# Kernel optimization log

Measured on AMD Instinct MI355X. Metric: run time of the kernel, lower is better.

The kernel has to match this reference:

```python
import jax, jax.numpy as jnp
import numpy as np

N, E, F_IN, HID, HEADS, C, NCLS, NG, NCONV = 50000, 800000, 128, 128, 8, 16, 10, 64, 3
EPS = 1e-5
NEG_SLOPE = 0.2


def bn_eval(x, p):
    # p: [4, dim] = (gamma, beta, running_mean, running_var); eval-mode BatchNorm1d
    g, b, m, v = p[0], p[1], p[2], p[3]
    return g * (x - m) * jax.lax.rsqrt(v + EPS) + b


def gat_conv(x, src, dst, W, a_src, a_dst, bias):
    # PyG GATConv, concat=True, add_self_loops=True, eval (no dropout)
    h = (x @ W).reshape(N, HEADS, C)                    # [N,H,C]
    alpha_s = jnp.sum(h * a_src[None], axis=-1)         # [N,H]
    alpha_d = jnp.sum(h * a_dst[None], axis=-1)         # [N,H]
    loop = jnp.arange(N)
    s = jnp.concatenate([src, loop])                    # [E+N]
    d = jnp.concatenate([dst, loop])
    logits = jax.nn.leaky_relu(alpha_s[s] + alpha_d[d], NEG_SLOPE)   # [E+N,H]
    mx = jax.lax.stop_gradient(jax.ops.segment_max(logits, d, num_segments=N))
    ex = jnp.exp(logits - mx[d])
    denom = jax.ops.segment_sum(ex, d, num_segments=N)
    alpha = ex / (denom[d] + 1e-16)                     # segment softmax over dst
    msg = h[s] * alpha[:, :, None]                      # [E+N,H,C]
    out = jax.ops.segment_sum(msg, d, num_segments=N)   # [N,H,C]
    return out.reshape(N, HEADS * C) + bias


def setup_inputs() -> dict:
    key = jax.random.key(0)
    ks = jax.random.split(key, 16)

    def bn_p(dim):
        return jnp.stack([jnp.ones(dim), jnp.full((dim,), 1e-4), jnp.zeros(dim), jnp.ones(dim)])

    sc = 0.05
    inp = {
        "x": jax.random.normal(ks[0], (N, F_IN), jnp.float32),
        "edge_index": jax.random.randint(ks[1], (2, E), 0, N),
        "batch": jnp.sort(jax.random.randint(ks[2], (N,), 0, NG)),
        "bn_feat_params": bn_p(F_IN),
        "w_feat": jax.random.normal(ks[3], (F_IN, HID), jnp.float32) * sc,
        "b_feat": jnp.zeros((HID,), jnp.float32),
        "bns_conv_params": jnp.stack([bn_p(HID)] * NCONV),
        "gat_w": jax.random.normal(ks[4], (NCONV, HID, HID), jnp.float32) * sc,
        "gat_att_src": jax.random.normal(ks[5], (NCONV, HEADS, C), jnp.float32) * sc,
        "gat_att_dst": jax.random.normal(ks[6], (NCONV, HEADS, C), jnp.float32) * sc,
        "gat_b": jnp.zeros((NCONV, HID), jnp.float32),
        "bns_fc_params": jnp.stack([bn_p(HID)] * 1),
        "fc_w": jax.random.normal(ks[7], (1, HID, HID), jnp.float32) * sc,
        "fc_b": jnp.zeros((1, HID), jnp.float32),
        "bn_hidden_params": bn_p(HID),
        "w_class": jax.random.normal(ks[8], (HID, NCLS), jnp.float32) * sc,
        "b_class": jnp.zeros((NCLS,), jnp.float32),
    }
    return inp


def reference(x, edge_index, batch, bn_feat_params, w_feat, b_feat, bns_conv_params,
              gat_w, gat_att_src, gat_att_dst, gat_b, bns_fc_params, fc_w, fc_b,
              bn_hidden_params, w_class, b_class):
    src, dst = edge_index[0], edge_index[1]
    h = bn_eval(x, bn_feat_params)
    h = jax.nn.relu(h @ w_feat + b_feat)             # GCNConv(gfn=True) == linear
    for i in range(NCONV):
        h = bn_eval(h, bns_conv_params[i])
        h = jax.nn.relu(gat_conv(h, src, dst, gat_w[i], gat_att_src[i], gat_att_dst[i], gat_b[i]))
    g = jax.ops.segment_sum(h, batch, num_segments=NG)   # global_add_pool -> [NG,HID]
    for i in range(fc_w.shape[0]):
        g = jax.nn.relu(bn_eval(g, bns_fc_params[i]) @ fc_w[i] + fc_b[i])
    g = bn_eval(g, bn_hidden_params)
    logits = g @ w_class + b_class
    return jax.nn.log_softmax(logits, axis=-1)
```

## Files before the change

kernel.cpp:

```cpp
#include <hip/hip_runtime.h>

#define NN 50000
#define E_EDGES 800000
#define F_INN 128
#define HIDD 128
#define HEADS 8
#define CDIM 16
#define NCLS 10
#define NGG 64
#define NCONV 3
#define EPSS 1e-5f
#define NEG_SLOPE 0.2f

#define WROWS 144
#define WSTRIDE (WROWS * 128)
#define BSTRIDE 144

#define BSH 7
#define BSZ 128
#define NB ((NN + BSZ - 1) / BSZ)
#define BIN_BLOCKS 256
#define BIN_CHUNK (E_EDGES / BIN_BLOCKS)
#define TABW 392
#define CAPB 4608
#define SORT_BUF 4608
#define PW_KCH 32
#define GTILES ((NN + 127) / 128)
#define TPITCH 132

typedef __attribute__((ext_vector_type(8))) short short8;
typedef __attribute__((ext_vector_type(4))) float f32x4;
typedef __attribute__((ext_vector_type(2))) float f32x2;

__device__ __forceinline__ float lrelu(float x) { return x > 0.f ? x : NEG_SLOPE * x; }

__device__ __forceinline__ float bf2f(ushort u) {
    union { unsigned int i; float f; } v;
    v.i = ((unsigned int)u) << 16;
    return v.f;
}
__device__ __forceinline__ ushort f2bf(float f) {
    union { float f; unsigned int i; } v;
    v.f = f;
    unsigned int r = (v.i + 0x7fffu + ((v.i >> 16) & 1u)) >> 16;
    return (ushort)r;
}
__device__ __forceinline__ unsigned char f2fp8(float f) {
    int r = __builtin_amdgcn_cvt_pk_fp8_f32(f, f, 0, false);
    return (unsigned char)(r & 0xff);
}

__device__ __forceinline__ void gemm_core_l0(int tile, int t,
    const float* __restrict__ Ain, const ushort* __restrict__ Wt,
    const float* __restrict__ bias, ushort* __restrict__ Out, int n)
{
    int wave = t >> 6, lane = t & 63;
    int m16 = lane & 15, quad = lane >> 4;
    int rbase = tile * 128 + wave * 32;

    short8 afrag[2][4];
    #pragma unroll
    for (int tt = 0; tt < 2; ++tt) {
        int arow_i = rbase + tt * 16 + m16;
        size_t arow = (size_t)(arow_i < n ? arow_i : 0) * HIDD + quad * 8;
        const float* ap = Ain + arow;
        #pragma unroll
        for (int kk = 0; kk < 4; ++kk) {
            float4 lo = *(const float4*)(ap + kk * 32);
            float4 hi = *(const float4*)(ap + kk * 32 + 4);
            short8 f;
            f[0] = (short)f2bf(lo.x); f[1] = (short)f2bf(lo.y);
            f[2] = (short)f2bf(lo.z); f[3] = (short)f2bf(lo.w);
            f[4] = (short)f2bf(hi.x); f[5] = (short)f2bf(hi.y);
            f[6] = (short)f2bf(hi.z); f[7] = (short)f2bf(hi.w);
            afrag[tt][kk] = f;
        }
    }

    f32x4 acc[2][8];
    #pragma unroll
    for (int tt = 0; tt < 2; ++tt)
        #pragma unroll
        for (int nt = 0; nt < 8; ++nt) acc[tt][nt] = (f32x4){0.f, 0.f, 0.f, 0.f};

    #pragma unroll
    for (int nt = 0; nt < 8; ++nt) {
        const ushort* brow = Wt + (size_t)(nt * 16 + m16) * HIDD + quad * 8;
        #pragma unroll
        for (int kk = 0; kk < 4; ++kk) {
            short8 bfrag = *(const short8*)(brow + kk * 32);
            acc[0][nt] = __builtin_amdgcn_mfma_f32_16x16x32_bf16(afrag[0][kk], bfrag, acc[0][nt], 0, 0, 0);
            acc[1][nt] = __builtin_amdgcn_mfma_f32_16x16x32_bf16(afrag[1][kk], bfrag, acc[1][nt], 0, 0, 0);
        }
    }

    #pragma unroll
    for (int tt = 0; tt < 2; ++tt) {
        int tb = rbase + tt * 16;
        #pragma unroll
        for (int nt = 0; nt < 8; ++nt) {
            int col = nt * 16 + m16;
            float bv = bias[col];
            #pragma unroll
            for (int r = 0; r < 4; ++r) {
                int orow = tb + quad * 4 + r;
                if (orow < n) {
                    float v = fmaxf(acc[tt][nt][r] + bv, 0.f);
                    Out[(size_t)orow * HIDD + col] = f2bf(v);
                }
            }
        }
    }
}

__global__ __launch_bounds__(256) void prep_bin(
    const float* __restrict__ bn_feat, const float* __restrict__ w_feat,
    const float* __restrict__ b_feat, const float* __restrict__ bns_conv,
    const float* __restrict__ gat_w, const float* __restrict__ att_src,
    const float* __restrict__ att_dst, const int* __restrict__ src,
    const int* __restrict__ dst, ushort* __restrict__ Wt,
    float* __restrict__ bp, unsigned int* __restrict__ tmp, int* __restrict__ tab)
{
    __shared__ __align__(16) char smem[18560];
    int blk = blockIdx.x;
    int t = threadIdx.x;

    if (blk < 16) {
        float* Wl = (float*)smem;
        float* aak = Wl + PW_KCH * 129;
        int layer = blk >> 2;
        int k0 = (blk & 3) * PW_KCH;
        const float* bn; const float* W;
        if (layer == 0) { bn = bn_feat; W = w_feat; }
        else { bn = bns_conv + (layer - 1) * 4 * HIDD; W = gat_w + (size_t)(layer - 1) * HIDD * HIDD; }
        if (t < PW_KCH) {
            int k = k0 + t;
            aak[t] = bn[k] * rsqrtf(bn[3 * HIDD + k] + EPSS);
        }
        for (int i = t; i < PW_KCH * 128; i += 256) {
            int kk = i >> 7, n = i & 127;
            Wl[kk * 129 + n] = W[(size_t)(k0 + kk) * 128 + n];
        }
        __syncthreads();
        ushort* wrow = Wt + (size_t)layer * WSTRIDE;
        for (int i = t; i < 128 * PW_KCH; i += 256) {
            int n = i >> 5, kk = i & 31;
            wrow[n * 128 + k0 + kk] = f2bf(aak[kk] * Wl[kk * 129 + n]);
        }
    } else if (blk < 20) {
        float* ccs = (float*)smem;
        int layer = blk - 16;
        const float* bn; const float* W;
        if (layer == 0) { bn = bn_feat; W = w_feat; }
        else { bn = bns_conv + (layer - 1) * 4 * HIDD; W = gat_w + (size_t)(layer - 1) * HIDD * HIDD; }
        if (t < 128) {
            float a = bn[t] * rsqrtf(bn[3 * HIDD + t] + EPSS);
            ccs[t] = bn[HIDD + t] - bn[2 * HIDD + t] * a;
        }
        __syncthreads();
        if (t < 128) {
            float bacc = (layer == 0) ? b_feat[t] : 0.f;
            for (int k = 0; k < 128; ++k) bacc += ccs[k] * W[(size_t)k * 128 + t];
            bp[layer * BSTRIDE + t] = bacc;
        }
    } else if (blk < 23) {
        float* Wl   = (float*)smem;
        float* redS = (float*)(smem + 16512);
        float* redD = redS + 256;
        int li = blk - 20;
        int L = li + 1;
        const float* bn = bns_conv + li * 4 * HIDD;
        const float* W  = gat_w + (size_t)li * HIDD * HIDD;
        const float* as = att_src + li * HEADS * CDIM;
        const float* ad = att_dst + li * HEADS * CDIM;
        ushort* Wo = Wt + (size_t)L * WSTRIDE;
        int kl = t >> 3, h = t & 7;
        float acc_s = 0.f, acc_d = 0.f;
        for (int c0 = 0; c0 < 4; ++c0) {
            int k0 = c0 * 32;
            __syncthreads();
            for (int i = t; i < 32 * 128; i += 256) {
                int kk = i >> 7, n = i & 127;
                Wl[kk * 129 + n] = W[(size_t)(k0 + kk) * 128 + n];
            }
            __syncthreads();
            int k = k0 + kl;
            float a  = bn[k] * rsqrtf(bn[3 * HIDD + k] + EPSS);
            float cc = bn[HIDD + k] - bn[2 * HIDD + k] * a;
            float ps = 0.f, pd = 0.f;
            #pragma unroll
            for (int c = 0; c < 16; ++c) {
                float wv = Wl[kl * 129 + h * 16 + c];
                ps += wv * as[h * 16 + c];
                pd += wv * ad[h * 16 + c];
            }
            Wo[(128 + h) * 128 + k] = f2bf(a * ps);
            Wo[(136 + h) * 128 + k] = f2bf(a * pd);
            acc_s += cc * ps;
            acc_d += cc * pd;
        }
        redS[t] = acc_s; redD[t] = acc_d;
        __syncthreads();
        if (t < 8) {
            float s = 0.f, d = 0.f;
            for (int q = 0; q < 32; ++q) { s += redS[q * 8 + t]; d += redD[q * 8 + t]; }
            bp[L * BSTRIDE + 128 + t] = s;
            bp[L * BSTRIDE + 136 + t] = d;
        }
    } else {
        unsigned int* stage = (unsigned int*)smem;
        int* hist = (int*)(smem + 12512);
        int* A    = hist + TABW;
        int k = blk - 23;
        int cbeg = k * BIN_CHUNK;
        int cend = cbeg + BIN_CHUNK;

        for (int i = t; i < TABW; i += 256) hist[i] = 0;
        __syncthreads();
        for (int e = cbeg + t; e < cend; e += 256)
            atomicAdd(&hist[dst[e] >> BSH], 1);
        __syncthreads();
        int i1 = t + 256;
        int c0 = hist[t];
        int c1 = (i1 < TABW) ? hist[i1] : 0;
        A[t] = c0; A[i1] = c1;
        __syncthreads();
        for (int d = 1; d < 512; d <<= 1) {
            int a0 = (t >= d) ? A[t - d] : 0;
            int a1 = A[i1 - d];
            __syncthreads();
            A[t] += a0; A[i1] += a1;
            __syncthreads();
        }
        int e0 = A[t] - c0;
        int e1 = A[i1] - c1;
        tab[(size_t)k * TABW + t] = e0;
        if (i1 < TABW) tab[(size_t)k * TABW + i1] = e1;
        hist[t] = e0;
        if (i1 < TABW) hist[i1] = e1;
        __syncthreads();
        for (int e = cbeg + t; e < cend; e += 256) {
            int d = dst[e];
            int b = d >> BSH;
            unsigned int pk = ((unsigned int)(d & (BSZ - 1)) << 16) | (unsigned int)src[e];
            int p = atomicAdd(&hist[b], 1);
            stage[p] = pk;
        }
        __syncthreads();
        for (int i = t; i < BIN_CHUNK; i += 256)
            tmp[(size_t)k * BIN_CHUNK + i] = stage[i];
    }
}

__global__ __launch_bounds__(256) void sort_gemm0(
    const int* __restrict__ tab, const unsigned int* __restrict__ tmp,
    ushort* __restrict__ csr, unsigned int* __restrict__ rowptr,
    const float* __restrict__ x, const ushort* __restrict__ Wt,
    const float* __restrict__ bp, ushort* __restrict__ h_a)
{
    int t = threadIdx.x;
    if (blockIdx.x < NB) {
        __shared__ unsigned int buf[SORT_BUF];
        __shared__ int sc[256];
        __shared__ int o0s[256];
        __shared__ int hist[BSZ], pex[BSZ], cur[BSZ];
        int b = blockIdx.x;
        int base_out = b * CAPB;

        int o0 = tab[(size_t)t * TABW + b];
        int o1 = tab[(size_t)t * TABW + b + 1];
        int c = o1 - o0;
        o0s[t] = o0;
        sc[t] = c;
        __syncthreads();
        for (int d = 1; d < 256; d <<= 1) {
            int a = (t >= d) ? sc[t - d] : 0;
            __syncthreads();
            sc[t] += a;
            __syncthreads();
        }
        int m = sc[255];
        int mybase = sc[t] - c;
        if (m > CAPB - BSZ * 7) m = CAPB - BSZ * 7;
        for (int j = 0; j < c; ++j) {
            int p = mybase + j;
            if (p < m) buf[p] = tmp[(size_t)t * BIN_CHUNK + o0s[t] + j];
        }
        if (t < BSZ) hist[t] = 0;
        __syncthreads();
        for (int i = t; i < m; i += 256) atomicAdd(&hist[buf[i] >> 16], 1);
        __syncthreads();
        int pd = 0;
        if (t < BSZ) { pd = (hist[t] + 7) & ~7; pex[t] = pd; }
        __syncthreads();
        for (int d = 1; d < BSZ; d <<= 1) {
            int a = (t < BSZ && t >= d) ? pex[t - d] : 0;
            __syncthreads();
            if (t < BSZ) pex[t] += a;
            __syncthreads();
        }
        if (t < BSZ) {
            int ex = pex[t] - pd;
            pex[t] = ex;
            cur[t] = ex;
            int node = b * BSZ + t;
            if (node < NN)
                rowptr[node] = (unsigned int)(base_out + ex) | ((unsigned int)hist[t] << 21);
        }
        __syncthreads();
        for (int i = t; i < m; i += 256) {
            unsigned int pk = buf[i];
            int dl = pk >> 16;
            int p = atomicAdd(&cur[dl], 1);
            csr[base_out + p] = (ushort)(pk & 0xffffu);
        }
        __syncthreads();
        if (t < BSZ) {
            int ex = pex[t], hn = hist[t], pdn = (hn + 7) & ~7;
            for (int i = hn; i < pdn; ++i) csr[base_out + ex + i] = 0;
        }
    } else {
        gemm_core_l0(blockIdx.x - NB, t, x, Wt, bp, h_a, NN);
    }
}

__global__ __launch_bounds__(256) void gemm_conv(const ushort* __restrict__ Ain,
    const ushort* __restrict__ Wt, const float* __restrict__ bias,
    unsigned char* __restrict__ h8, float* __restrict__ alph_s,
    float* __restrict__ alph_d)
{
    __shared__ unsigned char tile[128 * TPITCH];
    int t = threadIdx.x;
    int wave = t >> 6, lane = t & 63;
    int m16 = lane & 15, quad = lane >> 4;
    int tile0 = blockIdx.x * 128;
    int rbase = tile0 + wave * 32;
    const int n = NN;

    short8 afrag[2][4];
    #pragma unroll
    for (int tt = 0; tt < 2; ++tt) {
        int arow_i = rbase + tt * 16 + m16;
        size_t arow = (size_t)(arow_i < n ? arow_i : 0) * HIDD + quad * 8;
        const ushort* ap = Ain + arow;
        #pragma unroll
        for (int kk = 0; kk < 4; ++kk)
            afrag[tt][kk] = *(const short8*)(ap + kk * 32);
    }

    f32x4 acc[2][9];
    #pragma unroll
    for (int tt = 0; tt < 2; ++tt)
        #pragma unroll
        for (int nt = 0; nt < 9; ++nt) acc[tt][nt] = (f32x4){0.f, 0.f, 0.f, 0.f};

    #pragma unroll
    for (int nt = 0; nt < 9; ++nt) {
        const ushort* brow = Wt + (size_t)(nt * 16 + m16) * HIDD + quad * 8;
        #pragma unroll
        for (int kk = 0; kk < 4; ++kk) {
            short8 bfrag = *(const short8*)(brow + kk * 32);
            acc[0][nt] = __builtin_amdgcn_mfma_f32_16x16x32_bf16(afrag[0][kk], bfrag, acc[0][nt], 0, 0, 0);
            acc[1][nt] = __builtin_amdgcn_mfma_f32_16x16x32_bf16(afrag[1][kk], bfrag, acc[1][nt], 0, 0, 0);
        }
    }

    #pragma unroll
    for (int tt = 0; tt < 2; ++tt) {
        int lrow = wave * 32 + tt * 16;
        #pragma unroll
        for (int nt = 0; nt < 8; ++nt) {
            int col = nt * 16 + m16;
            float bv = bias[col];
            #pragma unroll
            for (int r = 0; r < 4; ++r) {
                float v = acc[tt][nt][r] + bv;
                tile[(lrow + quad * 4 + r) * TPITCH + col] = f2fp8(v);
            }
        }
        {
            float bv = bias[128 + m16];
            int tb = rbase + tt * 16;
            #pragma unroll
            for (int r = 0; r < 4; ++r) {
                int orow = tb + quad * 4 + r;
                if (orow < n) {
                    float v = acc[tt][8][r] + bv;
                    if (m16 < 8) alph_s[orow * HEADS + m16] = v;
                    else         alph_d[orow * HEADS + (m16 - 8)] = v;
                }
            }
        }
    }
    __syncthreads();
    {
        int row = t >> 1, half = t & 1;
        int orow = tile0 + row;
        if (orow < n) {
            const unsigned char* srcp = &tile[row * TPITCH + half * 64];
            uint4* dstp = (uint4*)(h8 + (size_t)orow * HIDD + half * 64);
            #pragma unroll
            for (int j = 0; j < 4; ++j)
                dstp[j] = *(const uint4*)(srcp + j * 16);
        }
    }
}

__global__ __launch_bounds__(256) void gat_aggregate(
    const unsigned char* __restrict__ h8,
    const float* __restrict__ as, const float* __restrict__ ad,
    const unsigned int* __restrict__ rowptr, const ushort* __restrict__ csr,
    const float* __restrict__ bias, ushort* __restrict__ out)
{
    int wid = (blockIdx.x * 256 + threadIdx.x) >> 6;
    int v = __builtin_amdgcn_readfirstlane(wid);
    if (v >= NN) return;
    int lane = threadIdx.x & 63;
    int hd = lane >> 3;
    int slot = lane & 7;
    int gbase = lane & ~7;
    unsigned int rp = rowptr[v];
    int beg = rp & 0x1FFFFF;
    int cnt = rp >> 21;
    float adv = ad[v * HEADS + hd];

    const ushort* h8v = (const ushort*)h8;

    float wself = __expf(lrelu(as[v * HEADS + hd] + adv));
    f32x2 sv = __builtin_amdgcn_cvt_pk_f32_fp8((int)h8v[(size_t)v * 64 + lane], false);
    float acc0 = wself * sv[0];
    float acc1 = wself * sv[1];
    float wsum_own = 0.f;

    int ngro = (cnt + 7) >> 3;
    if (ngro > 0) {
        const uint4* epk = (const uint4*)(csr + beg);
        int u0[8], u1[8];
        float l_own0, l_own1;
        unsigned int x0[8], x1[8];
        {
            uint4 pk = epk[0];
            u0[0] = pk.x & 0xffff; u0[1] = pk.x >> 16;
            u0[2] = pk.y & 0xffff; u0[3] = pk.y >> 16;
            u0[4] = pk.z & 0xffff; u0[5] = pk.z >> 16;
            u0[6] = pk.w & 0xffff; u0[7] = pk.w >> 16;
            unsigned int d = slot < 4 ? (slot < 2 ? pk.x : pk.y)
                                      : (slot < 6 ? pk.z : pk.w);
            int u_own = (slot & 1) ? (int)(d >> 16) : (int)(d & 0xffff);
            l_own0 = as[u_own * HEADS + hd];
            #pragma unroll
            for (int j = 0; j < 8; ++j) x0[j] = h8v[(size_t)u0[j] * 64 + lane];
        }
        for (int g = 0; g < ngro; ++g) {
            bool more = (g + 1 < ngro);
            if (more) {
                uint4 pk = epk[g + 1];
                u1[0] = pk.x & 0xffff; u1[1] = pk.x >> 16;
                u1[2] = pk.y & 0xffff; u1[3] = pk.y >> 16;
                u1[4] = pk.z & 0xffff; u1[5] = pk.z >> 16;
                u1[6] = pk.w & 0xffff; u1[7] = pk.w >> 16;
                unsigned int d = slot < 4 ? (slot < 2 ? pk.x : pk.y)
                                          : (slot < 6 ? pk.z : pk.w);
                int u_own = (slot & 1) ? (int)(d >> 16) : (int)(d & 0xffff);
                l_own1 = as[u_own * HEADS + hd];
                #pragma unroll
                for (int j = 0; j < 8; ++j) x1[j] = h8v[(size_t)u1[j] * 64 + lane];
            }
            float w_own = __expf(lrelu(l_own0 + adv));
            if (g * 8 + slot >= cnt) w_own = 0.f;
            wsum_own += w_own;
            #pragma unroll
            for (int j = 0; j < 8; ++j) {
                float wj = __shfl(w_own, gbase + j, 64);
                f32x2 hv2 = __builtin_amdgcn_cvt_pk_f32_fp8((int)x0[j], false);
                acc0 += wj * hv2[0];
                acc1 += wj * hv2[1];
            }
            if (more) {
                l_own0 = l_own1;
                #pragma unroll
                for (int j = 0; j < 8; ++j) { u0[j] = u1[j]; x0[j] = x1[j]; }
            }
        }
    }

    #pragma unroll
    for (int off = 1; off < 8; off <<= 1) wsum_own += __shfl_xor(wsum_own, off);
    float denom = wself + wsum_own;

    float inv = 1.f / (denom + 1e-16f);
    int c = 2 * lane;
    float o0 = fmaxf(acc0 * inv + bias[c], 0.f);
    float o1 = fmaxf(acc1 * inv + bias[c + 1], 0.f);
    ((unsigned int*)out)[(size_t)v * 64 + lane] =
        (unsigned int)f2bf(o0) | ((unsigned int)f2bf(o1) << 16);
}

__global__ __launch_bounds__(256) void pool_head(const ushort* __restrict__ h,
    const int* __restrict__ batch,
    const float* __restrict__ bns_fc, const float* __restrict__ fc_w,
    const float* __restrict__ fc_b, const float* __restrict__ bn_hid,
    const float* __restrict__ w_class, const float* __restrict__ b_class,
    float* __restrict__ out)
{
    __shared__ float sred[256];
    __shared__ float v1[HIDD];
    __shared__ float v2[HIDD];
    __shared__ float lg[NCLS];
    __shared__ float lse;
    __shared__ int bounds[2];
    int gb = blockIdx.x, t = threadIdx.x;

    if (t < 2) {
        int key = gb + t;
        int lo = 0, hi = NN;
        while (lo < hi) {
            int mid = (lo + hi) >> 1;
            if (batch[mid] < key) lo = mid + 1; else hi = mid;
        }
        bounds[t] = lo;
    }
    __syncthreads();
    int beg = bounds[0], end = bounds[1];

    int half = t >> 7, c = t & 127;
    float a0 = 0.f, a1 = 0.f, a2 = 0.f, a3 = 0.f;
    int r = beg + half;
    for (; r + 6 < end; r += 8) {
        a0 += bf2f(h[(size_t)r * HIDD + c]);
        a1 += bf2f(h[(size_t)(r + 2) * HIDD + c]);
        a2 += bf2f(h[(size_t)(r + 4) * HIDD + c]);
        a3 += bf2f(h[(size_t)(r + 6) * HIDD + c]);
    }
    for (; r < end; r += 2) a0 += bf2f(h[(size_t)r * HIDD + c]);
    sred[t] = (a0 + a1) + (a2 + a3);
    __syncthreads();

    if (t < HIDD) {
        float gv = sred[t] + sred[t + 128];
        float gamma = bns_fc[t], beta = bns_fc[HIDD + t];
        float mu = bns_fc[2 * HIDD + t], var = bns_fc[3 * HIDD + t];
        v1[t] = (gv - mu) * gamma * rsqrtf(var + EPSS) + beta;
    }
    __syncthreads();

    if (t < HIDD) {
        float acc = fc_b[t];
        for (int k = 0; k < HIDD; ++k) acc += v1[k] * fc_w[k * HIDD + t];
        acc = fmaxf(acc, 0.f);
        float gamma = bn_hid[t], beta = bn_hid[HIDD + t];
        float mu = bn_hid[2 * HIDD + t], var = bn_hid[3 * HIDD + t];
        v2[t] = (acc - mu) * gamma * rsqrtf(var + EPSS) + beta;
    }
    __syncthreads();

    if (t < NCLS) {
        float acc2 = b_class[t];
        for (int k = 0; k < HIDD; ++k) acc2 += v2[k] * w_class[k * NCLS + t];
        lg[t] = acc2;
    }
    __syncthreads();
    if (t == 0) {
        float mx = lg[0];
        for (int i = 1; i < NCLS; ++i) mx = fmaxf(mx, lg[i]);
        float ss = 0.f;
        for (int i = 0; i < NCLS; ++i) ss += __expf(lg[i] - mx);
        lse = mx + __logf(ss);
    }
    __syncthreads();
    if (t < NCLS) out[gb * NCLS + t] = lg[t] - lse;
}

extern "C" void kernel_launch(void* const* d_in, const int* in_sizes, int n_in,
                              void* d_out, int out_size, void* d_ws, size_t ws_size,
                              hipStream_t stream)
{
    const float* x        = (const float*)d_in[0];
    const int*   edge     = (const int*)d_in[1];
    const int*   batch    = (const int*)d_in[2];
    const float* bn_feat  = (const float*)d_in[3];
    const float* w_feat   = (const float*)d_in[4];
    const float* b_feat   = (const float*)d_in[5];
    const float* bns_conv = (const float*)d_in[6];
    const float* gat_w    = (const float*)d_in[7];
    const float* att_src  = (const float*)d_in[8];
    const float* att_dst  = (const float*)d_in[9];
    const float* gat_b    = (const float*)d_in[10];
    const float* bns_fc   = (const float*)d_in[11];
    const float* fc_w     = (const float*)d_in[12];
    const float* fc_b     = (const float*)d_in[13];
    const float* bn_hid   = (const float*)d_in[14];
    const float* w_class  = (const float*)d_in[15];
    const float* b_class  = (const float*)d_in[16];
    float* out = (float*)d_out;
    (void)in_sizes; (void)n_in; (void)out_size; (void)ws_size;

    char* ws = (char*)d_ws;
    size_t off = 0;
    auto alloc = [&](size_t bytes) {
        void* p = ws + off;
        off = (off + bytes + 255) & ~(size_t)255;
        return p;
    };
    ushort* Wt        = (ushort*)alloc((size_t)4 * WSTRIDE * sizeof(ushort));
    float*  bp        = (float*)alloc(4 * BSTRIDE * sizeof(float));
    ushort* h_a       = (ushort*)alloc((size_t)NN * HIDD * sizeof(ushort));
    unsigned char* h8 = (unsigned char*)alloc((size_t)NN * HIDD);
    float*  alph_s    = (float*)alloc((size_t)NN * HEADS * sizeof(float));
    float*  alph_d    = (float*)alloc((size_t)NN * HEADS * sizeof(float));
    int*    tab       = (int*)alloc((size_t)BIN_BLOCKS * TABW * sizeof(int));
    unsigned int* tmp = (unsigned int*)alloc((size_t)E_EDGES * sizeof(unsigned int));
    unsigned int* rowptr = (unsigned int*)alloc((size_t)NN * sizeof(unsigned int));
    ushort* csr       = (ushort*)alloc((size_t)NB * CAPB * sizeof(ushort) + 64);

    const int* src = edge;
    const int* dst = edge + E_EDGES;

    prep_bin<<<279, 256, 0, stream>>>(bn_feat, w_feat, b_feat, bns_conv, gat_w,
                                      att_src, att_dst, src, dst, Wt, bp, tmp, tab);
    sort_gemm0<<<NB + GTILES, 256, 0, stream>>>(tab, tmp, csr, rowptr,
                                                x, Wt, bp, h_a);

    for (int i = 0; i < NCONV; ++i) {
        gemm_conv<<<GTILES, 256, 0, stream>>>(h_a,
            Wt + (size_t)(i + 1) * WSTRIDE, bp + (i + 1) * BSTRIDE, h8,
            alph_s, alph_d);
        gat_aggregate<<<(NN + 3) / 4, 256, 0, stream>>>(h8, alph_s, alph_d,
                                                        rowptr, csr, gat_b + i * HIDD, h_a);
    }

    pool_head<<<NGG, 256, 0, stream>>>(h_a, batch, bns_fc, fc_w, fc_b, bn_hid,
                                       w_class, b_class, out);
}
```

Baseline: 313.2 us.

## Widen GAT gather to 32-bit loads, transpose bin table, vectorize pooling

The GAT aggregation now has each lane load 4 fp8 values (32 bits) per neighbor row instead of 2. The two wave halves each process alternate edges of every group of 8, and their partial sums are combined with a cross-half shuffle. This halves the number of gather load instructions per edge but adds shuffles and a final reduction. The bin offset table is transposed so the sort kernel reads it contiguously. Pooling now uses 16-byte vector loads with 16 row groups and a larger shared reduction.

```diff
diff --git a/kernel.cpp b/kernel.cpp
--- a/kernel.cpp
+++ b/kernel.cpp
@@ -234,8 +234,8 @@
         }
         int e0 = A[t] - c0;
         int e1 = A[i1] - c1;
-        tab[(size_t)k * TABW + t] = e0;
-        if (i1 < TABW) tab[(size_t)k * TABW + i1] = e1;
+        tab[(size_t)t * BIN_BLOCKS + k] = e0;
+        if (i1 < TABW) tab[(size_t)i1 * BIN_BLOCKS + k] = e1;
         hist[t] = e0;
         if (i1 < TABW) hist[i1] = e1;
         __syncthreads();
@@ -267,8 +267,8 @@
         int b = blockIdx.x;
         int base_out = b * CAPB;
 
-        int o0 = tab[(size_t)t * TABW + b];
-        int o1 = tab[(size_t)t * TABW + b + 1];
+        int o0 = tab[(size_t)b * BIN_BLOCKS + t];
+        int o1 = tab[(size_t)(b + 1) * BIN_BLOCKS + t];
         int c = o1 - o0;
         o0s[t] = o0;
         sc[t] = c;
@@ -418,68 +418,78 @@
     int lane = threadIdx.x & 63;
     int hd = lane >> 3;
     int slot = lane & 7;
-    int gbase = lane & ~7;
+    int half = lane >> 5;
+    int li = lane & 31;
+    int chh = li >> 2;
+
     unsigned int rp = rowptr[v];
     int beg = rp & 0x1FFFFF;
     int cnt = rp >> 21;
     float adv = ad[v * HEADS + hd];
 
-    const ushort* h8v = (const ushort*)h8;
+    const unsigned int* h32 = (const unsigned int*)h8;
 
     float wself = __expf(lrelu(as[v * HEADS + hd] + adv));
-    f32x2 sv = __builtin_amdgcn_cvt_pk_f32_fp8((int)h8v[(size_t)v * 64 + lane], false);
-    float acc0 = wself * sv[0];
-    float acc1 = wself * sv[1];
+    float wself_ch = __shfl(wself, chh * 8, 64);
+    unsigned int sx = h32[(size_t)v * 32 + li];
+    f32x2 sl = __builtin_amdgcn_cvt_pk_f32_fp8((int)sx, false);
+    f32x2 sh = __builtin_amdgcn_cvt_pk_f32_fp8((int)sx, true);
+    float selfm = half ? 0.f : wself_ch;
+    float acc0 = selfm * sl[0], acc1 = selfm * sl[1];
+    float acc2 = selfm * sh[0], acc3 = selfm * sh[1];
     float wsum_own = 0.f;
 
     int ngro = (cnt + 7) >> 3;
     if (ngro > 0) {
         const uint4* epk = (const uint4*)(csr + beg);
-        int u0[8], u1[8];
         float l_own0, l_own1;
-        unsigned int x0[8], x1[8];
+        int u0[4], u1[4];
+        unsigned int x0[4], x1[4];
         {
             uint4 pk = epk[0];
-            u0[0] = pk.x & 0xffff; u0[1] = pk.x >> 16;
-            u0[2] = pk.y & 0xffff; u0[3] = pk.y >> 16;
-            u0[4] = pk.z & 0xffff; u0[5] = pk.z >> 16;
-            u0[6] = pk.w & 0xffff; u0[7] = pk.w >> 16;
+            u0[0] = half ? (int)(pk.x >> 16) : (int)(pk.x & 0xffff);
+            u0[1] = half ? (int)(pk.y >> 16) : (int)(pk.y & 0xffff);
+            u0[2] = half ? (int)(pk.z >> 16) : (int)(pk.z & 0xffff);
+            u0[3] = half ? (int)(pk.w >> 16) : (int)(pk.w & 0xffff);
             unsigned int d = slot < 4 ? (slot < 2 ? pk.x : pk.y)
                                       : (slot < 6 ? pk.z : pk.w);
             int u_own = (slot & 1) ? (int)(d >> 16) : (int)(d & 0xffff);
             l_own0 = as[u_own * HEADS + hd];
             #pragma unroll
-            for (int j = 0; j < 8; ++j) x0[j] = h8v[(size_t)u0[j] * 64 + lane];
+            for (int j = 0; j < 4; ++j) x0[j] = h32[(size_t)u0[j] * 32 + li];
         }
         for (int g = 0; g < ngro; ++g) {
             bool more = (g + 1 < ngro);
             if (more) {
                 uint4 pk = epk[g + 1];
-                u1[0] = pk.x & 0xffff; u1[1] = pk.x >> 16;
-                u1[2] = pk.y & 0xffff; u1[3] = pk.y >> 16;
-                u1[4] = pk.z & 0xffff; u1[5] = pk.z >> 16;
-                u1[6] = pk.w & 0xffff; u1[7] = pk.w >> 16;
+                u1[0] = half ? (int)(pk.x >> 16) : (int)(pk.x & 0xffff);
+                u1[1] = half ? (int)(pk.y >> 16) : (int)(pk.y & 0xffff);
+                u1[2] = half ? (int)(pk.z >> 16) : (int)(pk.z & 0xffff);
+                u1[3] = half ? (int)(pk.w >> 16) : (int)(pk.w & 0xffff);
                 unsigned int d = slot < 4 ? (slot < 2 ? pk.x : pk.y)
                                           : (slot < 6 ? pk.z : pk.w);
                 int u_own = (slot & 1) ? (int)(d >> 16) : (int)(d & 0xffff);
                 l_own1 = as[u_own * HEADS + hd];
                 #pragma unroll
-                for (int j = 0; j < 8; ++j) x1[j] = h8v[(size_t)u1[j] * 64 + lane];
+                for (int j = 0; j < 4; ++j) x1[j] = h32[(size_t)u1[j] * 32 + li];
             }
             float w_own = __expf(lrelu(l_own0 + adv));
             if (g * 8 + slot >= cnt) w_own = 0.f;
             wsum_own += w_own;
             #pragma unroll
-            for (int j = 0; j < 8; ++j) {
-                float wj = __shfl(w_own, gbase + j, 64);
-                f32x2 hv2 = __builtin_amdgcn_cvt_pk_f32_fp8((int)x0[j], false);
-                acc0 += wj * hv2[0];
-                acc1 += wj * hv2[1];
+            for (int j = 0; j < 4; ++j) {
+                float wj = __shfl(w_own, chh * 8 + 2 * j + half, 64);
+                f32x2 lo = __builtin_amdgcn_cvt_pk_f32_fp8((int)x0[j], false);
+                f32x2 hi = __builtin_amdgcn_cvt_pk_f32_fp8((int)x0[j], true);
+                acc0 += wj * lo[0];
+                acc1 += wj * lo[1];
+                acc2 += wj * hi[0];
+                acc3 += wj * hi[1];
             }
             if (more) {
                 l_own0 = l_own1;
                 #pragma unroll
-                for (int j = 0; j < 8; ++j) { u0[j] = u1[j]; x0[j] = x1[j]; }
+                for (int j = 0; j < 4; ++j) { u0[j] = u1[j]; x0[j] = x1[j]; }
             }
         }
     }
@@ -487,12 +497,20 @@
     #pragma unroll
     for (int off = 1; off < 8; off <<= 1) wsum_own += __shfl_xor(wsum_own, off);
     float denom = wself + wsum_own;
-
-    float inv = 1.f / (denom + 1e-16f);
-    int c = 2 * lane;
-    float o0 = fmaxf(acc0 * inv + bias[c], 0.f);
-    float o1 = fmaxf(acc1 * inv + bias[c + 1], 0.f);
-    ((unsigned int*)out)[(size_t)v * 64 + lane] =
+    float inv_hd = 1.f / (denom + 1e-16f);
+    float inv = __shfl(inv_hd, chh * 8, 64);
+
+    acc0 += __shfl_xor(acc0, 32);
+    acc1 += __shfl_xor(acc1, 32);
+    acc2 += __shfl_xor(acc2, 32);
+    acc3 += __shfl_xor(acc3, 32);
+
+    float sa = half ? acc2 : acc0;
+    float sb = half ? acc3 : acc1;
+    int c0 = 4 * li + 2 * half;
+    float o0 = fmaxf(sa * inv + bias[c0], 0.f);
+    float o1 = fmaxf(sb * inv + bias[c0 + 1], 0.f);
+    ((unsigned int*)out)[(size_t)v * 64 + 2 * li + half] =
         (unsigned int)f2bf(o0) | ((unsigned int)f2bf(o1) << 16);
 }
 
@@ -503,7 +521,7 @@
     const float* __restrict__ w_class, const float* __restrict__ b_class,
     float* __restrict__ out)
 {
-    __shared__ float sred[256];
+    __shared__ float sred[2048];
     __shared__ float v1[HIDD];
     __shared__ float v2[HIDD];
     __shared__ float lg[NCLS];
@@ -523,21 +541,21 @@
     __syncthreads();
     int beg = bounds[0], end = bounds[1];
 
-    int half = t >> 7, c = t & 127;
-    float a0 = 0.f, a1 = 0.f, a2 = 0.f, a3 = 0.f;
-    int r = beg + half;
-    for (; r + 6 < end; r += 8) {
-        a0 += bf2f(h[(size_t)r * HIDD + c]);
-        a1 += bf2f(h[(size_t)(r + 2) * HIDD + c]);
-        a2 += bf2f(h[(size_t)(r + 4) * HIDD + c]);
-        a3 += bf2f(h[(size_t)(r + 6) * HIDD + c]);
-    }
-    for (; r < end; r += 2) a0 += bf2f(h[(size_t)r * HIDD + c]);
-    sred[t] = (a0 + a1) + (a2 + a3);
+    int rg = t >> 4, cg = t & 15;
+    float a[8] = {0.f, 0.f, 0.f, 0.f, 0.f, 0.f, 0.f, 0.f};
+    for (int r = beg + rg; r < end; r += 16) {
+        short8 vv = *(const short8*)(h + (size_t)r * HIDD + cg * 8);
+        #pragma unroll
+        for (int k = 0; k < 8; ++k) a[k] += bf2f((ushort)vv[k]);
+    }
+    #pragma unroll
+    for (int k = 0; k < 8; ++k) sred[rg * 128 + cg * 8 + k] = a[k];
     __syncthreads();
 
     if (t < HIDD) {
-        float gv = sred[t] + sred[t + 128];
+        float gv = 0.f;
+        #pragma unroll
+        for (int q = 0; q < 16; ++q) gv += sred[q * 128 + t];
         float gamma = bns_fc[t], beta = bns_fc[HIDD + t];
         float mu = bns_fc[2 * HIDD + t], var = bns_fc[3 * HIDD + t];
         v1[t] = (gv - mu) * gamma * rsqrtf(var + EPSS) + beta;
```

Measured after the change: 293.5 us (median of 3 runs). -6.3%, faster.
